# Optimization experiments

Measured on AMD Instinct MI355X. Metric: run time of the kernel, lower is better.

The kernel has to match this reference:

```python
import jax, jax.numpy as jnp
import numpy as np

NUM_NODES = 500000
DIM = 128
BATCH = 131072
MOMENTUM = 0.9


def setup_inputs() -> dict:
    key = jax.random.key(0)
    ks = jax.random.split(key, 6)
    s = 1.0 / np.sqrt(DIM)
    return {
        "hidden": jax.random.normal(ks[0], (NUM_NODES, DIM), jnp.float32),
        "variance": jnp.ones((NUM_NODES, DIM), jnp.float32),
        "idx": jnp.arange(BATCH, dtype=jnp.int64 if jax.config.jax_enable_x64 else jnp.int32),
        "new_repr": jax.random.normal(ks[1], (BATCH, DIM), jnp.float32),
        "W_ih": jax.random.normal(ks[2], (3 * DIM, DIM), jnp.float32) * s,
        "W_hh": jax.random.normal(ks[3], (3 * DIM, DIM), jnp.float32) * s,
        "b_ih": jax.random.normal(ks[4], (3 * DIM,), jnp.float32) * s,
        "b_hh": jax.random.normal(ks[5], (3 * DIM,), jnp.float32) * s,
    }


def _gru_cell(x, h, W_ih, W_hh, b_ih, b_hh):
    # torch GRUCell gate layout: [reset | update | new], each of size DIM
    gi = x @ W_ih.T + b_ih          # [B, 3*DIM]
    gh = h @ W_hh.T + b_hh          # [B, 3*DIM]
    gi_r, gi_z, gi_n = jnp.split(gi, 3, axis=-1)
    gh_r, gh_z, gh_n = jnp.split(gh, 3, axis=-1)
    r = jax.nn.sigmoid(gi_r + gh_r)
    z = jax.nn.sigmoid(gi_z + gh_z)
    n = jnp.tanh(gi_n + r * gh_n)
    return (1.0 - z) * n + z * h


def reference(hidden, variance, idx, new_repr, W_ih, W_hh, b_ih, b_hh):
    h_prev = hidden[idx]                                   # gather [B, DIM]
    h_new = _gru_cell(new_repr, h_prev, W_ih, W_hh, b_ih, b_hh)
    delta = h_new - h_prev
    var_new = MOMENTUM * variance[idx] + (1.0 - MOMENTUM) * delta * delta
    hidden_out = hidden.at[idx].set(h_new)                 # scatter write
    variance_out = variance.at[idx].set(var_new)
    return jnp.stack([hidden_out, variance_out])           # [2, N, DIM]
```

## Files before the change

kernel.cpp:

```cpp
#include <hip/hip_runtime.h>
#include <hip/hip_bf16.h>
#include <cstdint>
#include <cstddef>

#define NUM_NODES 500000
#define DIM 128
#define BATCH 131072

typedef __attribute__((ext_vector_type(8))) short short8;
typedef __attribute__((ext_vector_type(4))) short short4_t;
typedef __attribute__((ext_vector_type(4))) float f32x4;

static __device__ __forceinline__ short f2bf(float f) {
    unsigned u = __builtin_bit_cast(unsigned, f);
    u += 0x7fffu + ((u >> 16) & 1u);
    return (short)(u >> 16);
}
static __device__ __forceinline__ float bf2f(short s) {
    unsigned u = ((unsigned)(unsigned short)s) << 16;
    return __builtin_bit_cast(float, u);
}

__global__ void k_init(unsigned char* __restrict__ mask,
                       const float* __restrict__ Wih,
                       const float* __restrict__ Whh,
                       short* __restrict__ WbIH,
                       short* __restrict__ WbHH,
                       int do_mask) {
    int i = blockIdx.x * blockDim.x + threadIdx.x;
    if (do_mask && i < NUM_NODES) mask[i] = 0;
    if (i < 3 * DIM * DIM) {
        WbIH[i] = f2bf(Wih[i]);
        WbHH[i] = f2bf(Whh[i]);
    }
}

__global__ void k_scatter(unsigned char* __restrict__ mask, const int* __restrict__ idx) {
    int i = blockIdx.x * blockDim.x + threadIdx.x;
    if (i < BATCH) mask[idx[i]] = 1;
}

__global__ void __launch_bounds__(256)
k_copy(const float* __restrict__ hidden,
       const float* __restrict__ variance,
       const unsigned char* __restrict__ mask,
       float* __restrict__ out0,
       float* __restrict__ out1) {
    int gid = blockIdx.x * 256 + threadIdx.x;
    int row = gid >> 4;
    int c8  = gid & 15;
    if (mask && mask[row]) return;
    size_t off = (size_t)row * DIM + c8 * 8;
    f32x4 a0 = *(const f32x4*)(hidden + off);
    f32x4 a1 = *(const f32x4*)(hidden + off + 4);
    f32x4 b0 = *(const f32x4*)(variance + off);
    f32x4 b1 = *(const f32x4*)(variance + off + 4);
    *(f32x4*)(out0 + off)     = a0;
    *(f32x4*)(out0 + off + 4) = a1;
    *(f32x4*)(out1 + off)     = b0;
    *(f32x4*)(out1 + off + 4) = b1;
}

__global__ void __launch_bounds__(512)
k_gru(const float* __restrict__ hidden,
      const float* __restrict__ variance,
      const int*   __restrict__ idx,
      const float* __restrict__ xg,
      const short* __restrict__ WbIH,
      const short* __restrict__ WbHH,
      const float* __restrict__ b_ih,
      const float* __restrict__ b_hh,
      float* __restrict__ out0,
      float* __restrict__ out1) {
    __shared__ __align__(16) char smem[43008];
    short (*Xb)[136] = (short(*)[136])smem;
    short (*Hb)[136] = (short(*)[136])(smem + 8704);
    short (*Vb)[136] = (short(*)[136])(smem + 17408);
    float (*Hf)[132] = (float(*)[132])(smem + 26112);
    float (*Hn)[132] = (float(*)[132])smem;

    const int t  = threadIdx.x;
    const int rb = blockIdx.x * 32;

    for (int j = t; j < 1024; j += 512) {
        int row = j >> 5, c4 = j & 31;
        int node = idx[rb + row];
        f32x4 xv = *(const f32x4*)(xg + (size_t)(rb + row) * DIM + c4 * 4);
        f32x4 hv = *(const f32x4*)(hidden + (size_t)node * DIM + c4 * 4);
        f32x4 vv = *(const f32x4*)(variance + (size_t)node * DIM + c4 * 4);
        short4_t xs, hs, vs;
        xs.x = f2bf(xv.x); xs.y = f2bf(xv.y); xs.z = f2bf(xv.z); xs.w = f2bf(xv.w);
        hs.x = f2bf(hv.x); hs.y = f2bf(hv.y); hs.z = f2bf(hv.z); hs.w = f2bf(hv.w);
        vs.x = f2bf(vv.x); vs.y = f2bf(vv.y); vs.z = f2bf(vv.z); vs.w = f2bf(vv.w);
        *(short4_t*)&Xb[row][c4 * 4] = xs;
        *(short4_t*)&Hb[row][c4 * 4] = hs;
        *(short4_t*)&Vb[row][c4 * 4] = vs;
        *(f32x4*)&Hf[row][c4 * 4]    = hv;
    }
    __syncthreads();

    const int w  = t >> 6;
    const int l  = t & 63;
    const int c  = l & 15;
    const int gq = l >> 4;

    f32x4 acc[2][3][2] = {};

    #pragma unroll
    for (int ks = 0; ks < 4; ++ks) {
        const int k0 = ks * 32 + gq * 8;
        short8 a[2][2];
        a[0][0] = *(const short8*)&Xb[c][k0];
        a[1][0] = *(const short8*)&Xb[16 + c][k0];
        a[0][1] = *(const short8*)&Hb[c][k0];
        a[1][1] = *(const short8*)&Hb[16 + c][k0];
        #pragma unroll
        for (int th = 0; th < 3; ++th) {
            const int o = w * 16 + th * 128 + c;
            const short8 bi = *(const short8*)(WbIH + (size_t)o * DIM + k0);
            const short8 bh = *(const short8*)(WbHH + (size_t)o * DIM + k0);
            #pragma unroll
            for (int mt = 0; mt < 2; ++mt) {
                acc[mt][th][0] = __builtin_amdgcn_mfma_f32_16x16x32_bf16(a[mt][0], bi, acc[mt][th][0], 0, 0, 0);
                acc[mt][th][1] = __builtin_amdgcn_mfma_f32_16x16x32_bf16(a[mt][1], bh, acc[mt][th][1], 0, 0, 0);
            }
        }
    }

    __syncthreads();

    const int d = w * 16 + c;
    const float bs_r = b_ih[d]       + b_hh[d];
    const float bs_z = b_ih[d + 128] + b_hh[d + 128];
    const float bi_n = b_ih[d + 256];
    const float bh_n = b_hh[d + 256];

    #pragma unroll
    for (int mt = 0; mt < 2; ++mt) {
        #pragma unroll
        for (int r = 0; r < 4; ++r) {
            const int m = mt * 16 + gq * 4 + r;
            float s_r  = acc[mt][0][0][r] + acc[mt][0][1][r] + bs_r;
            float s_z  = acc[mt][1][0][r] + acc[mt][1][1][r] + bs_z;
            float gi_n = acc[mt][2][0][r] + bi_n;
            float gh_n = acc[mt][2][1][r] + bh_n;
            float rg = 1.f / (1.f + __expf(-s_r));
            float zg = 1.f / (1.f + __expf(-s_z));
            float aa = gi_n + rg * gh_n;
            float n  = 1.f - 2.f / (__expf(2.f * aa) + 1.f);
            float h  = Hf[m][d];
            Hn[m][d] = (1.f - zg) * n + zg * h;
        }
    }
    __syncthreads();

    for (int j = t; j < 1024; j += 512) {
        int row = j >> 5, c4 = j & 31;
        int node = idx[rb + row];
        size_t off = (size_t)node * DIM + c4 * 4;
        f32x4 hn = *(f32x4*)&Hn[row][c4 * 4];
        f32x4 h  = *(f32x4*)&Hf[row][c4 * 4];
        short4_t vs = *(short4_t*)&Vb[row][c4 * 4];
        f32x4 var;
        var.x = 0.9f * bf2f(vs.x) + 0.1f * (hn.x - h.x) * (hn.x - h.x);
        var.y = 0.9f * bf2f(vs.y) + 0.1f * (hn.y - h.y) * (hn.y - h.y);
        var.z = 0.9f * bf2f(vs.z) + 0.1f * (hn.z - h.z) * (hn.z - h.z);
        var.w = 0.9f * bf2f(vs.w) + 0.1f * (hn.w - h.w) * (hn.w - h.w);
        *(f32x4*)(out0 + off) = hn;
        *(f32x4*)(out1 + off) = var;
    }
}

extern "C" void kernel_launch(void* const* d_in, const int* in_sizes, int n_in,
                              void* d_out, int out_size, void* d_ws, size_t ws_size,
                              hipStream_t stream) {
    const float* hidden   = (const float*)d_in[0];
    const float* variance = (const float*)d_in[1];
    const int*   idx      = (const int*)d_in[2];
    const float* x        = (const float*)d_in[3];
    const float* Wih      = (const float*)d_in[4];
    const float* Whh      = (const float*)d_in[5];
    const float* bih      = (const float*)d_in[6];
    const float* bhh      = (const float*)d_in[7];
    float* out0 = (float*)d_out;
    float* out1 = out0 + (size_t)NUM_NODES * DIM;

    const size_t maskBytes = (size_t)NUM_NODES;
    const size_t wBytes    = (size_t)3 * DIM * DIM * 2;
    const bool   have_mask = ws_size >= maskBytes + 16 + 2 * wBytes;

    unsigned char* mask = have_mask ? (unsigned char*)d_ws : nullptr;
    short* WbIH = have_mask ? (short*)((char*)d_ws + ((maskBytes + 15) & ~size_t(15)))
                            : (short*)d_ws;
    short* WbHH = WbIH + 3 * DIM * DIM;

    k_init<<<(NUM_NODES + 255) / 256, 256, 0, stream>>>(
        mask ? mask : (unsigned char*)d_ws, Wih, Whh, WbIH, WbHH, have_mask ? 1 : 0);

    if (have_mask)
        k_scatter<<<BATCH / 256, 256, 0, stream>>>(mask, idx);

    k_copy<<<(NUM_NODES * 16) / 256, 256, 0, stream>>>(
        hidden, variance, mask, out0, out1);

    k_gru<<<BATCH / 32, 512, 0, stream>>>(hidden, variance, idx, x,
                                          WbIH, WbHH, bih, bhh, out0, out1);
}
```

Baseline: 288.6 us.

## Shrink GRU tiles to 16 rows with bf16-only LDS staging

The GRU kernel now handles 16 rows per block with 256 threads, and each wave covers 32 output columns across two N-tiles instead of two M-tiles. The fp32 copy of the previous hidden state and the fp32 new-hidden buffer are dropped from LDS, and both are kept in bf16 so shared memory falls from about 43KB to 13KB. Gate accumulators are computed one gate at a time to reduce register pressure and raise occupancy. In exchange, each weight fragment is reused across fewer rows, and the stored h_new and the previous hidden used for the blend and delta are now bf16-rounded, which adds precision loss.

```diff
diff --git a/kernel.cpp b/kernel.cpp
--- a/kernel.cpp
+++ b/kernel.cpp
@@ -61,7 +61,7 @@
     *(f32x4*)(out1 + off + 4) = b1;
 }
 
-__global__ void __launch_bounds__(512)
+__global__ void __launch_bounds__(256)
 k_gru(const float* __restrict__ hidden,
       const float* __restrict__ variance,
       const int*   __restrict__ idx,
@@ -72,17 +72,18 @@
       const float* __restrict__ b_hh,
       float* __restrict__ out0,
       float* __restrict__ out1) {
-    __shared__ __align__(16) char smem[43008];
+    __shared__ __align__(16) char smem[13056];
     short (*Xb)[136] = (short(*)[136])smem;
-    short (*Hb)[136] = (short(*)[136])(smem + 8704);
-    short (*Vb)[136] = (short(*)[136])(smem + 17408);
-    float (*Hf)[132] = (float(*)[132])(smem + 26112);
-    float (*Hn)[132] = (float(*)[132])smem;
+    short (*Hb)[136] = (short(*)[136])(smem + 4352);
+    short (*Vb)[136] = (short(*)[136])(smem + 8704);
+    short (*Hn)[136] = (short(*)[136])smem;
 
     const int t  = threadIdx.x;
-    const int rb = blockIdx.x * 32;
-
-    for (int j = t; j < 1024; j += 512) {
+    const int rb = blockIdx.x * 16;
+
+    #pragma unroll
+    for (int jj = 0; jj < 2; ++jj) {
+        int j = t + jj * 256;
         int row = j >> 5, c4 = j & 31;
         int node = idx[rb + row];
         f32x4 xv = *(const f32x4*)(xg + (size_t)(rb + row) * DIM + c4 * 4);
@@ -95,7 +96,6 @@
         *(short4_t*)&Xb[row][c4 * 4] = xs;
         *(short4_t*)&Hb[row][c4 * 4] = hs;
         *(short4_t*)&Vb[row][c4 * 4] = vs;
-        *(f32x4*)&Hf[row][c4 * 4]    = hv;
     }
     __syncthreads();
 
@@ -104,68 +104,73 @@
     const int c  = l & 15;
     const int gq = l >> 4;
 
-    f32x4 acc[2][3][2] = {};
-
-    #pragma unroll
-    for (int ks = 0; ks < 4; ++ks) {
-        const int k0 = ks * 32 + gq * 8;
-        short8 a[2][2];
-        a[0][0] = *(const short8*)&Xb[c][k0];
-        a[1][0] = *(const short8*)&Xb[16 + c][k0];
-        a[0][1] = *(const short8*)&Hb[c][k0];
-        a[1][1] = *(const short8*)&Hb[16 + c][k0];
+    float s_r[2][4], s_z[2][4], gin[2][4], ghn[2][4];
+
+    #pragma unroll
+    for (int th = 0; th < 3; ++th) {
+        f32x4 acc[2][2] = {};
         #pragma unroll
-        for (int th = 0; th < 3; ++th) {
-            const int o = w * 16 + th * 128 + c;
-            const short8 bi = *(const short8*)(WbIH + (size_t)o * DIM + k0);
-            const short8 bh = *(const short8*)(WbHH + (size_t)o * DIM + k0);
+        for (int ks = 0; ks < 4; ++ks) {
+            const int k0 = ks * 32 + gq * 8;
+            const short8 aX = *(const short8*)&Xb[c][k0];
+            const short8 aH = *(const short8*)&Hb[c][k0];
             #pragma unroll
-            for (int mt = 0; mt < 2; ++mt) {
-                acc[mt][th][0] = __builtin_amdgcn_mfma_f32_16x16x32_bf16(a[mt][0], bi, acc[mt][th][0], 0, 0, 0);
-                acc[mt][th][1] = __builtin_amdgcn_mfma_f32_16x16x32_bf16(a[mt][1], bh, acc[mt][th][1], 0, 0, 0);
+            for (int nt = 0; nt < 2; ++nt) {
+                const int o = th * 128 + w * 32 + nt * 16 + c;
+                const short8 bi = *(const short8*)(WbIH + (size_t)o * DIM + k0);
+                const short8 bh = *(const short8*)(WbHH + (size_t)o * DIM + k0);
+                acc[nt][0] = __builtin_amdgcn_mfma_f32_16x16x32_bf16(aX, bi, acc[nt][0], 0, 0, 0);
+                acc[nt][1] = __builtin_amdgcn_mfma_f32_16x16x32_bf16(aH, bh, acc[nt][1], 0, 0, 0);
             }
         }
-    }
-
+        #pragma unroll
+        for (int nt = 0; nt < 2; ++nt)
+            #pragma unroll
+            for (int r = 0; r < 4; ++r) {
+                if (th == 0) s_r[nt][r] = acc[nt][0][r] + acc[nt][1][r];
+                if (th == 1) s_z[nt][r] = acc[nt][0][r] + acc[nt][1][r];
+                if (th == 2) { gin[nt][r] = acc[nt][0][r]; ghn[nt][r] = acc[nt][1][r]; }
+            }
+    }
     __syncthreads();
 
-    const int d = w * 16 + c;
-    const float bs_r = b_ih[d]       + b_hh[d];
-    const float bs_z = b_ih[d + 128] + b_hh[d + 128];
-    const float bi_n = b_ih[d + 256];
-    const float bh_n = b_hh[d + 256];
-
-    #pragma unroll
-    for (int mt = 0; mt < 2; ++mt) {
+    #pragma unroll
+    for (int nt = 0; nt < 2; ++nt) {
+        const int d = w * 32 + nt * 16 + c;
+        const float bsr = b_ih[d]       + b_hh[d];
+        const float bsz = b_ih[d + 128] + b_hh[d + 128];
+        const float bin = b_ih[d + 256];
+        const float bhn = b_hh[d + 256];
         #pragma unroll
         for (int r = 0; r < 4; ++r) {
-            const int m = mt * 16 + gq * 4 + r;
-            float s_r  = acc[mt][0][0][r] + acc[mt][0][1][r] + bs_r;
-            float s_z  = acc[mt][1][0][r] + acc[mt][1][1][r] + bs_z;
-            float gi_n = acc[mt][2][0][r] + bi_n;
-            float gh_n = acc[mt][2][1][r] + bh_n;
-            float rg = 1.f / (1.f + __expf(-s_r));
-            float zg = 1.f / (1.f + __expf(-s_z));
-            float aa = gi_n + rg * gh_n;
+            const int m = gq * 4 + r;
+            float rg = 1.f / (1.f + __expf(-(s_r[nt][r] + bsr)));
+            float zg = 1.f / (1.f + __expf(-(s_z[nt][r] + bsz)));
+            float aa = (gin[nt][r] + bin) + rg * (ghn[nt][r] + bhn);
             float n  = 1.f - 2.f / (__expf(2.f * aa) + 1.f);
-            float h  = Hf[m][d];
-            Hn[m][d] = (1.f - zg) * n + zg * h;
+            float h  = bf2f(Hb[m][d]);
+            Hn[m][d] = f2bf((1.f - zg) * n + zg * h);
         }
     }
     __syncthreads();
 
-    for (int j = t; j < 1024; j += 512) {
+    #pragma unroll
+    for (int jj = 0; jj < 2; ++jj) {
+        int j = t + jj * 256;
         int row = j >> 5, c4 = j & 31;
         int node = idx[rb + row];
         size_t off = (size_t)node * DIM + c4 * 4;
-        f32x4 hn = *(f32x4*)&Hn[row][c4 * 4];
-        f32x4 h  = *(f32x4*)&Hf[row][c4 * 4];
-        short4_t vs = *(short4_t*)&Vb[row][c4 * 4];
-        f32x4 var;
-        var.x = 0.9f * bf2f(vs.x) + 0.1f * (hn.x - h.x) * (hn.x - h.x);
-        var.y = 0.9f * bf2f(vs.y) + 0.1f * (hn.y - h.y) * (hn.y - h.y);
-        var.z = 0.9f * bf2f(vs.z) + 0.1f * (hn.z - h.z) * (hn.z - h.z);
-        var.w = 0.9f * bf2f(vs.w) + 0.1f * (hn.w - h.w) * (hn.w - h.w);
+        short4_t hns = *(short4_t*)&Hn[row][c4 * 4];
+        short4_t hs  = *(short4_t*)&Hb[row][c4 * 4];
+        short4_t vs  = *(short4_t*)&Vb[row][c4 * 4];
+        f32x4 hn, var;
+        hn.x = bf2f(hns.x); hn.y = bf2f(hns.y); hn.z = bf2f(hns.z); hn.w = bf2f(hns.w);
+        float dx = hn.x - bf2f(hs.x), dy = hn.y - bf2f(hs.y);
+        float dz = hn.z - bf2f(hs.z), dw = hn.w - bf2f(hs.w);
+        var.x = 0.9f * bf2f(vs.x) + 0.1f * dx * dx;
+        var.y = 0.9f * bf2f(vs.y) + 0.1f * dy * dy;
+        var.z = 0.9f * bf2f(vs.z) + 0.1f * dz * dz;
+        var.w = 0.9f * bf2f(vs.w) + 0.1f * dw * dw;
         *(f32x4*)(out0 + off) = hn;
         *(f32x4*)(out1 + off) = var;
     }
@@ -203,6 +208,6 @@
     k_copy<<<(NUM_NODES * 16) / 256, 256, 0, stream>>>(
         hidden, variance, mask, out0, out1);
 
-    k_gru<<<BATCH / 32, 512, 0, stream>>>(hidden, variance, idx, x,
+    k_gru<<<BATCH / 16, 256, 0, stream>>>(hidden, variance, idx, x,
                                           WbIH, WbHH, bih, bhh, out0, out1);
 }
```

Result: slower. 381.9 us (+32.3%).

## Fuse copy and GRU update into one node-ordered streaming kernel via inverse index map

Applied to the files above, without the earlier changes.

Builds an inverse map from node to batch position, then launches one kernel over all node blocks. Each block either copies its rows straight through or, when any row is updated, reads hidden and variance contiguously, gathers x through the inverse map, runs the GRU MFMA and writes results. This removes the separate copy pass and the random-access gather and scatter, so hidden and variance are read once instead of twice for updated rows. The new hidden and the delta used for the variance update are now stored in bf16, which adds rounding error to the outputs. Duplicate indices resolve to the last writer in the inverse map, and the old path is kept as a fallback when workspace is small.

```diff
diff --git a/kernel.cpp b/kernel.cpp
--- a/kernel.cpp
+++ b/kernel.cpp
@@ -6,6 +6,7 @@
 #define NUM_NODES 500000
 #define DIM 128
 #define BATCH 131072
+#define NBLK (NUM_NODES / 32)
 
 typedef __attribute__((ext_vector_type(8))) short short8;
 typedef __attribute__((ext_vector_type(4))) short short4_t;
@@ -21,23 +22,173 @@
     return __builtin_bit_cast(float, u);
 }
 
-__global__ void k_init(unsigned char* __restrict__ mask,
+__global__ void k_init(int* __restrict__ inv,
+                       unsigned char* __restrict__ mask,
                        const float* __restrict__ Wih,
                        const float* __restrict__ Whh,
                        short* __restrict__ WbIH,
-                       short* __restrict__ WbHH,
-                       int do_mask) {
+                       short* __restrict__ WbHH) {
     int i = blockIdx.x * blockDim.x + threadIdx.x;
-    if (do_mask && i < NUM_NODES) mask[i] = 0;
+    if (i < NUM_NODES) {
+        if (inv)  inv[i] = -1;
+        if (mask) mask[i] = 0;
+    }
     if (i < 3 * DIM * DIM) {
         WbIH[i] = f2bf(Wih[i]);
         WbHH[i] = f2bf(Whh[i]);
     }
 }
 
-__global__ void k_scatter(unsigned char* __restrict__ mask, const int* __restrict__ idx) {
+__global__ void k_scatter(int* __restrict__ inv, unsigned char* __restrict__ mask,
+                          const int* __restrict__ idx) {
     int i = blockIdx.x * blockDim.x + threadIdx.x;
-    if (i < BATCH) mask[idx[i]] = 1;
+    if (i < BATCH) {
+        int n = idx[i];
+        if (inv)  inv[n] = i;
+        if (mask) mask[n] = 1;
+    }
+}
+
+__global__ void __launch_bounds__(512)
+k_stream(const float* __restrict__ hidden,
+         const float* __restrict__ variance,
+         const int*   __restrict__ inv,
+         const float* __restrict__ xg,
+         const short* __restrict__ WbIH,
+         const short* __restrict__ WbHH,
+         const float* __restrict__ b_ih,
+         const float* __restrict__ b_hh,
+         float* __restrict__ out0,
+         float* __restrict__ out1) {
+    __shared__ __align__(16) char smem[26112];
+    short (*Xb)[136] = (short(*)[136])smem;
+    short (*Hb)[136] = (short(*)[136])(smem + 8704);
+    short (*Vb)[136] = (short(*)[136])(smem + 17408);
+    short (*Hn)[136] = (short(*)[136])smem;
+    __shared__ int rinfo[32];
+    __shared__ int hasUpd;
+
+    const int t  = threadIdx.x;
+    const int rb = blockIdx.x * 32;
+
+    if (t == 0) hasUpd = 0;
+    if (t < 32) rinfo[t] = inv[rb + t];
+    __syncthreads();
+    if (t < 32 && rinfo[t] >= 0) hasUpd = 1;
+    __syncthreads();
+
+    if (!hasUpd) {
+        #pragma unroll
+        for (int jj = 0; jj < 2; ++jj) {
+            int j = t + jj * 512;
+            size_t off = (size_t)rb * DIM + j * 4;
+            f32x4 h = *(const f32x4*)(hidden + off);
+            f32x4 v = *(const f32x4*)(variance + off);
+            *(f32x4*)(out0 + off) = h;
+            *(f32x4*)(out1 + off) = v;
+        }
+        return;
+    }
+
+    #pragma unroll
+    for (int jj = 0; jj < 2; ++jj) {
+        int j = t + jj * 512;
+        int row = j >> 5, c4 = j & 31;
+        size_t off = (size_t)(rb + row) * DIM + c4 * 4;
+        f32x4 hv = *(const f32x4*)(hidden + off);
+        f32x4 vv = *(const f32x4*)(variance + off);
+        int iv = rinfo[row];
+        f32x4 xv = {0.f, 0.f, 0.f, 0.f};
+        if (iv >= 0) {
+            xv = *(const f32x4*)(xg + (size_t)iv * DIM + c4 * 4);
+        } else {
+            *(f32x4*)(out0 + off) = hv;
+            *(f32x4*)(out1 + off) = vv;
+        }
+        short4_t xs, hs, vs;
+        xs.x = f2bf(xv.x); xs.y = f2bf(xv.y); xs.z = f2bf(xv.z); xs.w = f2bf(xv.w);
+        hs.x = f2bf(hv.x); hs.y = f2bf(hv.y); hs.z = f2bf(hv.z); hs.w = f2bf(hv.w);
+        vs.x = f2bf(vv.x); vs.y = f2bf(vv.y); vs.z = f2bf(vv.z); vs.w = f2bf(vv.w);
+        *(short4_t*)&Xb[row][c4 * 4] = xs;
+        *(short4_t*)&Hb[row][c4 * 4] = hs;
+        *(short4_t*)&Vb[row][c4 * 4] = vs;
+    }
+    __syncthreads();
+
+    const int w  = t >> 6;
+    const int l  = t & 63;
+    const int c  = l & 15;
+    const int gq = l >> 4;
+
+    f32x4 acc[2][3][2] = {};
+
+    #pragma unroll
+    for (int ks = 0; ks < 4; ++ks) {
+        const int k0 = ks * 32 + gq * 8;
+        short8 a[2][2];
+        a[0][0] = *(const short8*)&Xb[c][k0];
+        a[1][0] = *(const short8*)&Xb[16 + c][k0];
+        a[0][1] = *(const short8*)&Hb[c][k0];
+        a[1][1] = *(const short8*)&Hb[16 + c][k0];
+        #pragma unroll
+        for (int th = 0; th < 3; ++th) {
+            const int o = w * 16 + th * 128 + c;
+            const short8 bi = *(const short8*)(WbIH + (size_t)o * DIM + k0);
+            const short8 bh = *(const short8*)(WbHH + (size_t)o * DIM + k0);
+            #pragma unroll
+            for (int mt = 0; mt < 2; ++mt) {
+                acc[mt][th][0] = __builtin_amdgcn_mfma_f32_16x16x32_bf16(a[mt][0], bi, acc[mt][th][0], 0, 0, 0);
+                acc[mt][th][1] = __builtin_amdgcn_mfma_f32_16x16x32_bf16(a[mt][1], bh, acc[mt][th][1], 0, 0, 0);
+            }
+        }
+    }
+    __syncthreads();
+
+    const int d = w * 16 + c;
+    const float bs_r = b_ih[d]       + b_hh[d];
+    const float bs_z = b_ih[d + 128] + b_hh[d + 128];
+    const float bi_n = b_ih[d + 256];
+    const float bh_n = b_hh[d + 256];
+
+    #pragma unroll
+    for (int mt = 0; mt < 2; ++mt) {
+        #pragma unroll
+        for (int r = 0; r < 4; ++r) {
+            const int m = mt * 16 + gq * 4 + r;
+            float s_r  = acc[mt][0][0][r] + acc[mt][0][1][r] + bs_r;
+            float s_z  = acc[mt][1][0][r] + acc[mt][1][1][r] + bs_z;
+            float gi_n = acc[mt][2][0][r] + bi_n;
+            float gh_n = acc[mt][2][1][r] + bh_n;
+            float rg = 1.f / (1.f + __expf(-s_r));
+            float zg = 1.f / (1.f + __expf(-s_z));
+            float aa = gi_n + rg * gh_n;
+            float n  = 1.f - 2.f / (__expf(2.f * aa) + 1.f);
+            float h  = bf2f(Hb[m][d]);
+            Hn[m][d] = f2bf((1.f - zg) * n + zg * h);
+        }
+    }
+    __syncthreads();
+
+    #pragma unroll
+    for (int jj = 0; jj < 2; ++jj) {
+        int j = t + jj * 512;
+        int row = j >> 5, c4 = j & 31;
+        if (rinfo[row] < 0) continue;
+        size_t off = (size_t)(rb + row) * DIM + c4 * 4;
+        short4_t hns = *(short4_t*)&Hn[row][c4 * 4];
+        short4_t hs  = *(short4_t*)&Hb[row][c4 * 4];
+        short4_t vs  = *(short4_t*)&Vb[row][c4 * 4];
+        f32x4 hn, var;
+        hn.x = bf2f(hns.x); hn.y = bf2f(hns.y); hn.z = bf2f(hns.z); hn.w = bf2f(hns.w);
+        float dx = hn.x - bf2f(hs.x), dy = hn.y - bf2f(hs.y);
+        float dz = hn.z - bf2f(hs.z), dw = hn.w - bf2f(hs.w);
+        var.x = 0.9f * bf2f(vs.x) + 0.1f * dx * dx;
+        var.y = 0.9f * bf2f(vs.y) + 0.1f * dy * dy;
+        var.z = 0.9f * bf2f(vs.z) + 0.1f * dz * dz;
+        var.w = 0.9f * bf2f(vs.w) + 0.1f * dw * dw;
+        *(f32x4*)(out0 + off) = hn;
+        *(f32x4*)(out1 + off) = var;
+    }
 }
 
 __global__ void __launch_bounds__(256)
@@ -72,17 +223,18 @@
       const float* __restrict__ b_hh,
       float* __restrict__ out0,
       float* __restrict__ out1) {
-    __shared__ __align__(16) char smem[43008];
+    __shared__ __align__(16) char smem[26112];
     short (*Xb)[136] = (short(*)[136])smem;
     short (*Hb)[136] = (short(*)[136])(smem + 8704);
     short (*Vb)[136] = (short(*)[136])(smem + 17408);
-    float (*Hf)[132] = (float(*)[132])(smem + 26112);
-    float (*Hn)[132] = (float(*)[132])smem;
+    short (*Hn)[136] = (short(*)[136])smem;
 
     const int t  = threadIdx.x;
     const int rb = blockIdx.x * 32;
 
-    for (int j = t; j < 1024; j += 512) {
+    #pragma unroll
+    for (int jj = 0; jj < 2; ++jj) {
+        int j = t + jj * 512;
         int row = j >> 5, c4 = j & 31;
         int node = idx[rb + row];
         f32x4 xv = *(const f32x4*)(xg + (size_t)(rb + row) * DIM + c4 * 4);
@@ -95,7 +247,6 @@
         *(short4_t*)&Xb[row][c4 * 4] = xs;
         *(short4_t*)&Hb[row][c4 * 4] = hs;
         *(short4_t*)&Vb[row][c4 * 4] = vs;
-        *(f32x4*)&Hf[row][c4 * 4]    = hv;
     }
     __syncthreads();
 
@@ -105,7 +256,6 @@
     const int gq = l >> 4;
 
     f32x4 acc[2][3][2] = {};
-
     #pragma unroll
     for (int ks = 0; ks < 4; ++ks) {
         const int k0 = ks * 32 + gq * 8;
@@ -126,7 +276,6 @@
             }
         }
     }
-
     __syncthreads();
 
     const int d = w * 16 + c;
@@ -134,7 +283,6 @@
     const float bs_z = b_ih[d + 128] + b_hh[d + 128];
     const float bi_n = b_ih[d + 256];
     const float bh_n = b_hh[d + 256];
-
     #pragma unroll
     for (int mt = 0; mt < 2; ++mt) {
         #pragma unroll
@@ -148,24 +296,29 @@
             float zg = 1.f / (1.f + __expf(-s_z));
             float aa = gi_n + rg * gh_n;
             float n  = 1.f - 2.f / (__expf(2.f * aa) + 1.f);
-            float h  = Hf[m][d];
-            Hn[m][d] = (1.f - zg) * n + zg * h;
-        }
-    }
-    __syncthreads();
-
-    for (int j = t; j < 1024; j += 512) {
+            float h  = bf2f(Hb[m][d]);
+            Hn[m][d] = f2bf((1.f - zg) * n + zg * h);
+        }
+    }
+    __syncthreads();
+
+    #pragma unroll
+    for (int jj = 0; jj < 2; ++jj) {
+        int j = t + jj * 512;
         int row = j >> 5, c4 = j & 31;
         int node = idx[rb + row];
         size_t off = (size_t)node * DIM + c4 * 4;
-        f32x4 hn = *(f32x4*)&Hn[row][c4 * 4];
-        f32x4 h  = *(f32x4*)&Hf[row][c4 * 4];
-        short4_t vs = *(short4_t*)&Vb[row][c4 * 4];
-        f32x4 var;
-        var.x = 0.9f * bf2f(vs.x) + 0.1f * (hn.x - h.x) * (hn.x - h.x);
-        var.y = 0.9f * bf2f(vs.y) + 0.1f * (hn.y - h.y) * (hn.y - h.y);
-        var.z = 0.9f * bf2f(vs.z) + 0.1f * (hn.z - h.z) * (hn.z - h.z);
-        var.w = 0.9f * bf2f(vs.w) + 0.1f * (hn.w - h.w) * (hn.w - h.w);
+        short4_t hns = *(short4_t*)&Hn[row][c4 * 4];
+        short4_t hs  = *(short4_t*)&Hb[row][c4 * 4];
+        short4_t vs  = *(short4_t*)&Vb[row][c4 * 4];
+        f32x4 hn, var;
+        hn.x = bf2f(hns.x); hn.y = bf2f(hns.y); hn.z = bf2f(hns.z); hn.w = bf2f(hns.w);
+        float dx = hn.x - bf2f(hs.x), dy = hn.y - bf2f(hs.y);
+        float dz = hn.z - bf2f(hs.z), dw = hn.w - bf2f(hs.w);
+        var.x = 0.9f * bf2f(vs.x) + 0.1f * dx * dx;
+        var.y = 0.9f * bf2f(vs.y) + 0.1f * dy * dy;
+        var.z = 0.9f * bf2f(vs.z) + 0.1f * dz * dz;
+        var.w = 0.9f * bf2f(vs.w) + 0.1f * dw * dw;
         *(f32x4*)(out0 + off) = hn;
         *(f32x4*)(out1 + off) = var;
     }
@@ -185,24 +338,41 @@
     float* out0 = (float*)d_out;
     float* out1 = out0 + (size_t)NUM_NODES * DIM;
 
-    const size_t maskBytes = (size_t)NUM_NODES;
-    const size_t wBytes    = (size_t)3 * DIM * DIM * 2;
-    const bool   have_mask = ws_size >= maskBytes + 16 + 2 * wBytes;
-
-    unsigned char* mask = have_mask ? (unsigned char*)d_ws : nullptr;
-    short* WbIH = have_mask ? (short*)((char*)d_ws + ((maskBytes + 15) & ~size_t(15)))
-                            : (short*)d_ws;
-    short* WbHH = WbIH + 3 * DIM * DIM;
-
-    k_init<<<(NUM_NODES + 255) / 256, 256, 0, stream>>>(
-        mask ? mask : (unsigned char*)d_ws, Wih, Whh, WbIH, WbHH, have_mask ? 1 : 0);
-
-    if (have_mask)
-        k_scatter<<<BATCH / 256, 256, 0, stream>>>(mask, idx);
-
-    k_copy<<<(NUM_NODES * 16) / 256, 256, 0, stream>>>(
-        hidden, variance, mask, out0, out1);
-
-    k_gru<<<BATCH / 32, 512, 0, stream>>>(hidden, variance, idx, x,
-                                          WbIH, WbHH, bih, bhh, out0, out1);
-}
+    const size_t invB  = (size_t)NUM_NODES * 4;
+    const size_t maskB = (size_t)NUM_NODES;
+    const size_t wB    = (size_t)3 * DIM * DIM * 2;
+
+    const bool full = ws_size >= invB + 2 * wB;
+    const bool mid  = !full && ws_size >= maskB + 16 + 2 * wB;
+
+    if (full) {
+        int*   inv  = (int*)d_ws;
+        short* WbIH = (short*)((char*)d_ws + invB);
+        short* WbHH = WbIH + 3 * DIM * DIM;
+        k_init<<<(NUM_NODES + 255) / 256, 256, 0, stream>>>(
+            inv, nullptr, Wih, Whh, WbIH, WbHH);
+        k_scatter<<<BATCH / 256, 256, 0, stream>>>(inv, nullptr, idx);
+        k_stream<<<NBLK, 512, 0, stream>>>(hidden, variance, inv, x,
+                                           WbIH, WbHH, bih, bhh, out0, out1);
+    } else if (mid) {
+        unsigned char* mask = (unsigned char*)d_ws;
+        short* WbIH = (short*)((char*)d_ws + ((maskB + 15) & ~size_t(15)));
+        short* WbHH = WbIH + 3 * DIM * DIM;
+        k_init<<<(NUM_NODES + 255) / 256, 256, 0, stream>>>(
+            nullptr, mask, Wih, Whh, WbIH, WbHH);
+        k_scatter<<<BATCH / 256, 256, 0, stream>>>(nullptr, mask, idx);
+        k_copy<<<(NUM_NODES * 16) / 256, 256, 0, stream>>>(
+            hidden, variance, mask, out0, out1);
+        k_gru<<<BATCH / 32, 512, 0, stream>>>(hidden, variance, idx, x,
+                                              WbIH, WbHH, bih, bhh, out0, out1);
+    } else {
+        short* WbIH = (short*)d_ws;
+        short* WbHH = WbIH + 3 * DIM * DIM;
+        k_init<<<(NUM_NODES + 255) / 256, 256, 0, stream>>>(
+            nullptr, nullptr, Wih, Whh, WbIH, WbHH);
+        k_copy<<<(NUM_NODES * 16) / 256, 256, 0, stream>>>(
+            hidden, variance, nullptr, out0, out1);
+        k_gru<<<BATCH / 32, 512, 0, stream>>>(hidden, variance, idx, x,
+                                              WbIH, WbHH, bih, bhh, out0, out1);
+    }
+}
```

Result: faster. 267.3 us (-7.4%).
